# Optimization experiments

Hardware: AMD Instinct MI355X
Metric: run time of the kernel (lower is better)

## Reference

```python
import jax, jax.numpy as jnp
import numpy as np

N = 16384      # nodes
DEG = 20       # avg degree
E = N * DEG    # edges
MUL = 8        # multiplicity of 0e and 1o irreps
NB = 10        # number_of_basis
HID = 64       # fc hidden size
RMAX = 3.5     # max_radius
WNUM = 4 * MUL * MUL  # tp weight numel (4 parity-allowed paths)


def setup_inputs() -> dict:
    key = jax.random.key(0)
    ks = jax.random.split(key, 12)
    f = jax.random.normal(ks[0], (N, 4 * MUL), dtype=jnp.float32)  # 8 scalars + 8 vectors (3 comps)
    pos = jax.random.uniform(ks[1], (N, 3), dtype=jnp.float32) * 2.0  # box keeps dists < RMAX
    rng = np.random.default_rng(0)
    edge_dst = np.repeat(np.arange(N), DEG)
    edge_src = rng.integers(0, N, size=E)
    edge_src = np.where(edge_src == edge_dst, (edge_src + 1) % N, edge_src)
    return {
        'f': f, 'pos': pos,
        'Wq_s': jax.random.normal(ks[2], (MUL, MUL), jnp.float32),
        'Wq_v': jax.random.normal(ks[3], (MUL, MUL), jnp.float32),
        'Wk1': jax.random.normal(ks[4], (NB, HID), jnp.float32),
        'Wk2': jax.random.normal(ks[5], (HID, WNUM), jnp.float32),
        'Wv1': jax.random.normal(ks[6], (NB, HID), jnp.float32),
        'Wv2': jax.random.normal(ks[7], (HID, WNUM), jnp.float32),
        'Wd_s': jax.random.normal(ks[8], (MUL, MUL), jnp.float32),
        'Wd_v': jax.random.normal(ks[9], (MUL, MUL), jnp.float32),
        'edge_src': jnp.asarray(edge_src, jnp.int32),
        'edge_dst': jnp.asarray(edge_dst, jnp.int32),
    }


def _soft_unit_step(x):
    # e3nn soft_unit_step: exp(-1/x) for x>0 else 0; safe for grads
    xs = jnp.where(x > 0, x, 1.0)
    return jnp.where(x > 0, jnp.exp(-1.0 / xs), 0.0)


def _split(x):
    # [*, 4*MUL] -> scalars [*, MUL], vectors [*, MUL, 3]
    return x[:, :MUL], x[:, MUL:].reshape(-1, MUL, 3)


def _fc(x, W1, W2):
    # e3nn FullyConnectedNet: normalized linear -> act -> normalized linear
    h = jax.nn.silu(x @ W1 / jnp.sqrt(jnp.float32(NB)))
    return h @ W2 / jnp.sqrt(jnp.float32(HID))


def _tp(xs, xv, s0, s1, w):
    # fully connected tensor product (in: MULx0e+MULx1o) x (1x0e+1x1o) -> MULx0e+MULx1o
    # w: [E, 4, MUL, MUL]; paths: ss->s, vv->s (dot/sqrt3), sv->v, vs->v
    norm = 1.0 / (MUL ** 0.5 * 2.0 ** 0.5)
    out_s = (jnp.einsum('ei,eio->eo', xs * s0[:, None], w[:, 0]) +
             jnp.einsum('eic,ec,eio->eo', xv, s1, w[:, 1]) / 3.0 ** 0.5) * norm
    out_v = (jnp.einsum('ei,ec,eio->eoc', xs, s1, w[:, 2]) +
             jnp.einsum('eic,eio->eoc', xv * s0[:, None, None], w[:, 3])) * norm
    return out_s, out_v


def reference(f, pos, Wq_s, Wq_v, Wk1, Wk2, Wv1, Wv2, Wd_s, Wd_v, edge_src, edge_dst):
    edge_vec = pos[edge_src] - pos[edge_dst]                      # [E,3]
    r = jnp.linalg.norm(edge_vec, axis=1)                         # [E]
    # soft_one_hot_linspace, basis='smooth_finite', cutoff=True
    values = jnp.linspace(0.0, RMAX, NB + 2)[1:-1]
    step = RMAX / (NB + 1)
    d = (r[:, None] - values) / step
    basis = (1.14136 * np.exp(2.0)) * _soft_unit_step(d + 1.0) * _soft_unit_step(1.0 - d)
    emb = basis * NB ** 0.5                                       # [E,NB]
    cutoff = _soft_unit_step(10.0 * (1.0 - r / RMAX))             # [E]
    # spherical harmonics l=0,1; normalize=True, 'component' norm
    unit = edge_vec / r[:, None]
    s0 = jnp.ones_like(r)
    s1 = (3.0 ** 0.5) * unit                                      # [E,3]
    # query (equivariant linear per irrep)
    fs, fv = _split(f)
    qs = fs @ Wq_s / MUL ** 0.5                                   # [N,MUL]
    qv = jnp.einsum('eic,io->eoc', fv, Wq_v) / MUL ** 0.5         # [N,MUL,3]
    # per-edge tp weights from radial net
    wk = _fc(emb, Wk1, Wk2).reshape(E, 4, MUL, MUL)
    wv = _fc(emb, Wv1, Wv2).reshape(E, 4, MUL, MUL)
    gs, gv = fs[edge_src], fv[edge_src]                           # gather
    ks_, kv_ = _tp(gs, gv, s0, s1, wk)
    vs_, vv_ = _tp(gs, gv, s0, s1, wv)
    # dot tp (q x k -> 0e), shared weights
    qds, qdv = qs[edge_dst], qv[edge_dst]
    logits = (jnp.einsum('ei,ej,ij->e', qds, ks_, Wd_s) +
              jnp.einsum('eic,ejc,ij->e', qdv, kv_, Wd_v) / 3.0 ** 0.5) / (MUL * 2.0 ** 0.5)
    # scatter softmax with cutoff weighting
    mx = jax.ops.segment_max(logits, edge_dst, num_segments=N)
    mx = jnp.where(jnp.isneginf(mx), 0.0, mx)
    expw = cutoff * jnp.exp(logits - mx[edge_dst])
    z = jax.ops.segment_sum(expw, edge_dst, num_segments=N)
    z = jnp.where(z == 0, 1.0, z)
    alpha = expw / z[edge_dst]
    coef = jnp.sqrt(jax.nn.relu(alpha) + 1e-12)                   # [E]
    out_s = jax.ops.segment_sum(coef[:, None] * vs_, edge_dst, num_segments=N)
    out_v = jax.ops.segment_sum(coef[:, None, None] * vv_, edge_dst, num_segments=N)
    return jnp.concatenate([out_s, out_v.reshape(N, 3 * MUL)], axis=1)
```

## Files before the change

### kernel.cpp

```cpp
#include <hip/hip_runtime.h>
#include <hip/hip_bf16.h>
#include <math.h>

#define NN 16384
#define DEG 20
#define EE (NN*DEG)
#define RMAXF 3.5f
#define NGRP 5

typedef __attribute__((ext_vector_type(8))) short short8;
typedef __attribute__((ext_vector_type(4))) float f32x4;

__device__ __forceinline__ float su_f(float x) {
    return x > 0.0f ? __expf(-__builtin_amdgcn_rcpf(x)) : 0.0f;
}
__device__ __forceinline__ ushort f2bf(float x) {
    __hip_bfloat16 h = __float2bfloat16(x);
    return *reinterpret_cast<ushort*>(&h);
}
__device__ __forceinline__ float bf2f(ushort u) {
    return __uint_as_float(((unsigned int)u) << 16);
}

__global__ __launch_bounds__(256, 3) void edge_kernel(
    const float* __restrict__ f,   const float* __restrict__ pos,
    const float* __restrict__ Wqs, const float* __restrict__ Wqv,
    const float* __restrict__ Wds, const float* __restrict__ Wdv,
    const float* __restrict__ Wk1, const float* __restrict__ Wv1,
    const float* __restrict__ Wk2, const float* __restrict__ Wv2,
    const int* __restrict__ esrc,  float* __restrict__ out)
{
    __shared__ float  s_w[2][16][260];
    __shared__ __align__(16) ushort s_hb[2][16][64];
    __shared__ __align__(16) float s_g[2][16][36];
    __shared__ float s_emb[2][16][10];
    __shared__ float s_s1[2][16][4];
    __shared__ float s_b[16][9];
    __shared__ __align__(4) ushort s_v[80][34];
    __shared__ float s_lg[80];
    __shared__ float s_cut[80];
    __shared__ float s_mqn[4][32];
    __shared__ int   s_esrc[80];

    const int t = threadIdx.x;
    const int wave = t >> 6, lane = t & 63;
    const int qd = lane >> 4, n = lane & 15;
    const int n0 = blockIdx.x * 4;
    const int E0 = n0 * DEG;

    if (t < 128) {
        int nd = t >> 5, idx = t & 31;
        const float* fr = f + (size_t)(n0 + nd) * 32;
        const float inv8 = 0.35355339059327373f;
        float o_ = 0.0f;
        if (idx < 8) {
            int j = idx;
            #pragma unroll
            for (int i = 0; i < 8; i++) {
                float qs = 0.0f;
                #pragma unroll
                for (int a = 0; a < 8; a++) qs = fmaf(fr[a], Wqs[a * 8 + i], qs);
                o_ = fmaf(qs * inv8, Wds[i * 8 + j], o_);
            }
        } else {
            int kk = idx - 8;
            int j = kk / 3, c = kk - 3 * j;
            #pragma unroll
            for (int i = 0; i < 8; i++) {
                float qv = 0.0f;
                #pragma unroll
                for (int a = 0; a < 8; a++) qv = fmaf(fr[8 + 3 * a + c], Wqv[a * 8 + i], qv);
                o_ = fmaf(qv * inv8, Wdv[i * 8 + j], o_);
            }
            o_ *= 0.5773502691896258f;
        }
        s_mqn[nd][idx] = o_;
    }
    if (t < 80) s_esrc[t] = esrc[E0 + t];
    __syncthreads();

    float wk1r[10], wv1r[10];
    #pragma unroll
    for (int j = 0; j < 10; j++) {
        wk1r[j] = Wk1[j * 64 + lane];
        wv1r[j] = Wv1[j * 64 + lane];
    }

    short8 breg[2][2][4];
    #pragma unroll
    for (int net = 0; net < 2; net++) {
        const float* W2 = net ? Wv2 : Wk2;
        #pragma unroll
        for (int s = 0; s < 2; s++)
            #pragma unroll
            for (int jj = 0; jj < 4; jj++) {
                int col = (wave * 4 + jj) * 16 + n;
                union { ushort u[8]; short8 v; } bf;
                #pragma unroll
                for (int j = 0; j < 8; j++) {
                    int k0 = s * 32 + qd * 8 + j;
                    bf.u[j] = f2bf(W2[k0 * 256 + col] * 0.125f);
                }
                breg[net][s][jj] = bf.v;
            }
    }

    {
        int e = t >> 4, rl = t & 15;
        if (rl < 11) {
            int s = s_esrc[e];
            int d = n0;
            float vx = pos[s * 3 + 0] - pos[d * 3 + 0];
            float vy = pos[s * 3 + 1] - pos[d * 3 + 1];
            float vz = pos[s * 3 + 2] - pos[d * 3 + 2];
            float r = sqrtf(vx * vx + vy * vy + vz * vz);
            if (rl < 10) {
                const float step = RMAXF / 11.0f;
                const float invstep = 11.0f / RMAXF;
                const float K = 26.66929988626f;
                float dd = (r - step * (float)(rl + 1)) * invstep;
                s_emb[0][e][rl] = K * su_f(dd + 1.0f) * su_f(1.0f - dd);
            } else {
                float invr = __builtin_amdgcn_rcpf(r);
                const float sqrt3 = 1.7320508075688772f;
                s_s1[0][e][0] = sqrt3 * vx * invr;
                s_s1[0][e][1] = sqrt3 * vy * invr;
                s_s1[0][e][2] = sqrt3 * vz * invr;
                s_cut[e] = su_f(10.0f * (1.0f - r / RMAXF));
            }
        }
        if (t < 128) {
            int el = t >> 3, c4 = t & 7;
            int s = s_esrc[el];
            float4 x = *reinterpret_cast<const float4*>(f + (size_t)s * 32 + c4 * 4);
            *reinterpret_cast<float4*>(&s_g[0][el][c4 * 4]) = x;
        }
    }
    __syncthreads();

    for (int g = 0; g < NGRP; g++) {
        const int cb = g & 1, nbuf = cb ^ 1;
        const int le0 = g * 16;
        const bool more = (g + 1 < NGRP);

        float psx = 0.f, psy = 0.f, psz = 0.f, pdx = 0.f, pdy = 0.f, pdz = 0.f;
        float4 pf4 = {0.f, 0.f, 0.f, 0.f};
        {
            int e = t >> 4, rl = t & 15;
            if (more && rl < 11) {
                int s = s_esrc[le0 + 16 + e];
                int d = n0 + (le0 + 16 + e) / DEG;
                psx = pos[s * 3 + 0]; psy = pos[s * 3 + 1]; psz = pos[s * 3 + 2];
                pdx = pos[d * 3 + 0]; pdy = pos[d * 3 + 1]; pdz = pos[d * 3 + 2];
            }
            if (more && t < 128) {
                int el = t >> 3, c4 = t & 7;
                int s = s_esrc[le0 + 16 + el];
                pf4 = *reinterpret_cast<const float4*>(f + (size_t)s * 32 + c4 * 4);
            }
        }

        {
            const float invsq10 = 0.31622776601683794f;
            #pragma unroll
            for (int e = 0; e < 4; e++) {
                int el = wave * 4 + e;
                float ak = 0.0f, av = 0.0f;
                #pragma unroll
                for (int j = 0; j < 10; j++) {
                    float ej = s_emb[cb][el][j];
                    ak = fmaf(ej, wk1r[j], ak);
                    av = fmaf(ej, wv1r[j], av);
                }
                ak *= invsq10; av *= invsq10;
                float hk = ak * __builtin_amdgcn_rcpf(1.0f + __expf(-ak));
                float hv = av * __builtin_amdgcn_rcpf(1.0f + __expf(-av));
                int pos_ = ((((lane >> 3) ^ (el & 7))) << 3) | (lane & 7);
                s_hb[0][el][pos_] = f2bf(hk);
                s_hb[1][el][pos_] = f2bf(hv);
            }
            if (t < 128) {
                int el = t >> 3, k = t & 7;
                const float inv_sqrt3 = 0.5773502691896258f;
                s_b[el][k] = (s_g[cb][el][8 + 3 * k + 0] * s_s1[cb][el][0] +
                              s_g[cb][el][8 + 3 * k + 1] * s_s1[cb][el][1] +
                              s_g[cb][el][8 + 3 * k + 2] * s_s1[cb][el][2]) * inv_sqrt3;
            }
        }

        if (more) {
            int e = t >> 4, rl = t & 15;
            if (rl < 11) {
                float vx = psx - pdx, vy = psy - pdy, vz = psz - pdz;
                float r = sqrtf(vx * vx + vy * vy + vz * vz);
                if (rl < 10) {
                    const float step = RMAXF / 11.0f;
                    const float invstep = 11.0f / RMAXF;
                    const float K = 26.66929988626f;
                    float dd = (r - step * (float)(rl + 1)) * invstep;
                    s_emb[nbuf][e][rl] = K * su_f(dd + 1.0f) * su_f(1.0f - dd);
                } else {
                    float invr = __builtin_amdgcn_rcpf(r);
                    const float sqrt3 = 1.7320508075688772f;
                    s_s1[nbuf][e][0] = sqrt3 * vx * invr;
                    s_s1[nbuf][e][1] = sqrt3 * vy * invr;
                    s_s1[nbuf][e][2] = sqrt3 * vz * invr;
                    s_cut[le0 + 16 + e] = su_f(10.0f * (1.0f - r / RMAXF));
                }
            }
            if (t < 128) {
                int el = t >> 3, c4 = t & 7;
                *reinterpret_cast<float4*>(&s_g[nbuf][el][c4 * 4]) = pf4;
            }
        }
        __syncthreads();

        #pragma unroll
        for (int net = 0; net < 2; net++) {
            short8 ha0 = *(const short8*)&s_hb[net][n][((qd ^ (n & 7)) << 3)];
            short8 ha1 = *(const short8*)&s_hb[net][n][(((4 + qd) ^ (n & 7)) << 3)];
            #pragma unroll
            for (int jj = 0; jj < 4; jj++) {
                int tt = wave * 4 + jj;
                f32x4 d = {0.0f, 0.0f, 0.0f, 0.0f};
                d = __builtin_amdgcn_mfma_f32_16x16x32_bf16(ha0, breg[net][0][jj], d, 0, 0, 0);
                d = __builtin_amdgcn_mfma_f32_16x16x32_bf16(ha1, breg[net][1][jj], d, 0, 0, 0);
                #pragma unroll
                for (int r = 0; r < 4; r++)
                    s_w[net][4 * qd + r][tt * 16 + n] = d[r];
            }
        }
        __syncthreads();

        {
            int u = t & 127;
            int el = u >> 3, o = u & 7;
            int le = le0 + el;
            float g_[32];
            #pragma unroll
            for (int v4 = 0; v4 < 8; v4++) {
                float4 x = *reinterpret_cast<const float4*>(&s_g[cb][el][v4 * 4]);
                g_[v4 * 4 + 0] = x.x; g_[v4 * 4 + 1] = x.y;
                g_[v4 * 4 + 2] = x.z; g_[v4 * 4 + 3] = x.w;
            }
            const float nrm = 0.25f;

            if (t < 128) {
                int nd = le / DEG;
                const float* wk = s_w[0][el];
                float ks = 0.0f, uk = 0.0f;
                #pragma unroll
                for (int i = 0; i < 8; i++) {
                    ks += g_[i] * wk[i * 8 + o] + s_b[el][i] * wk[64 + i * 8 + o];
                    uk = fmaf(g_[i], wk[128 + i * 8 + o], uk);
                }
                float contrib = s_mqn[nd][o] * (ks * nrm);
                #pragma unroll
                for (int c = 0; c < 3; c++) {
                    float tk = 0.0f;
                    #pragma unroll
                    for (int i = 0; i < 8; i++)
                        tk = fmaf(g_[8 + 3 * i + c], wk[192 + i * 8 + o], tk);
                    float kv_c = nrm * (s_s1[cb][el][c] * uk + tk);
                    contrib = fmaf(s_mqn[nd][8 + 3 * o + c], kv_c, contrib);
                }
                contrib += __shfl_xor(contrib, 1);
                contrib += __shfl_xor(contrib, 2);
                contrib += __shfl_xor(contrib, 4);
                if (o == 0) s_lg[le] = contrib * 0.08838834764831845f;
            } else {
                const float* wv = s_w[1][el];
                float vs = 0.0f, uv = 0.0f;
                #pragma unroll
                for (int i = 0; i < 8; i++) {
                    vs += g_[i] * wv[i * 8 + o] + s_b[el][i] * wv[64 + i * 8 + o];
                    uv = fmaf(g_[i], wv[128 + i * 8 + o], uv);
                }
                s_v[le][o] = f2bf(vs * nrm);
                #pragma unroll
                for (int c = 0; c < 3; c++) {
                    float tv = 0.0f;
                    #pragma unroll
                    for (int i = 0; i < 8; i++)
                        tv = fmaf(g_[8 + 3 * i + c], wv[192 + i * 8 + o], tv);
                    s_v[le][8 + 3 * o + c] = f2bf(nrm * (s_s1[cb][el][c] * uv + tv));
                }
            }
        }
        __syncthreads();
    }

    {
        int base_le = DEG * wave;
        int h32 = lane & 32;
        int hl = lane & 31;
        float lg = -INFINITY, cw = 0.0f;
        if (hl < DEG) {
            lg = s_lg[base_le + hl];
            cw = s_cut[base_le + hl];
        }
        float mx = lg;
        mx = fmaxf(mx, __shfl_xor(mx, 16));
        mx = fmaxf(mx, __shfl_xor(mx, 8));
        mx = fmaxf(mx, __shfl_xor(mx, 4));
        mx = fmaxf(mx, __shfl_xor(mx, 2));
        mx = fmaxf(mx, __shfl_xor(mx, 1));

        float ew = cw * __expf(lg - mx);
        float z = ew;
        z += __shfl_xor(z, 16);
        z += __shfl_xor(z, 8);
        z += __shfl_xor(z, 4);
        z += __shfl_xor(z, 2);
        z += __shfl_xor(z, 1);
        z = (z == 0.0f) ? 1.0f : z;
        float coef = sqrtf(ew * __builtin_amdgcn_rcpf(z) + 1e-12f);

        float acc = 0.0f;
        #pragma unroll
        for (int ee = 0; ee < DEG; ee++) {
            float ce = __shfl(coef, h32 + ee);
            acc = fmaf(ce, bf2f(s_v[base_le + ee][hl]), acc);
        }
        if (lane < 32) out[(size_t)(n0 + wave) * 32 + hl] = acc;
    }
}

extern "C" void kernel_launch(void* const* d_in, const int* in_sizes, int n_in,
                              void* d_out, int out_size, void* d_ws, size_t ws_size,
                              hipStream_t stream) {
    const float* f    = (const float*)d_in[0];
    const float* pos  = (const float*)d_in[1];
    const float* Wqs  = (const float*)d_in[2];
    const float* Wqv  = (const float*)d_in[3];
    const float* Wk1  = (const float*)d_in[4];
    const float* Wk2  = (const float*)d_in[5];
    const float* Wv1  = (const float*)d_in[6];
    const float* Wv2  = (const float*)d_in[7];
    const float* Wds  = (const float*)d_in[8];
    const float* Wdv  = (const float*)d_in[9];
    const int* esrc   = (const int*)d_in[10];
    float* out        = (float*)d_out;

    edge_kernel<<<dim3(NN / 4), dim3(256), 0, stream>>>(
        f, pos, Wqs, Wqv, Wds, Wdv, Wk1, Wv1, Wk2, Wv2, esrc, out);
}
```

Baseline: 177.8 us.

## Deepen the edge-group software pipeline and drop one barrier per group

Result: slower. 195.4 us (+9.9%).

```diff
diff --git a/kernel.cpp b/kernel.cpp
--- a/kernel.cpp
+++ b/kernel.cpp
@@ -138,56 +138,64 @@
     }
     __syncthreads();
 
+    float psx = 0.f, psy = 0.f, psz = 0.f, pdx = 0.f, pdy = 0.f, pdz = 0.f;
+    float4 pf4 = {0.f, 0.f, 0.f, 0.f};
+    {
+        int e = t >> 4, rl = t & 15;
+        if (rl < 11) {
+            int s = s_esrc[16 + e];
+            int d = n0 + (16 + e) / DEG;
+            psx = pos[s * 3 + 0]; psy = pos[s * 3 + 1]; psz = pos[s * 3 + 2];
+            pdx = pos[d * 3 + 0]; pdy = pos[d * 3 + 1]; pdz = pos[d * 3 + 2];
+        }
+        if (t < 128) {
+            int el = t >> 3, c4 = t & 7;
+            int s = s_esrc[16 + el];
+            pf4 = *reinterpret_cast<const float4*>(f + (size_t)s * 32 + c4 * 4);
+        }
+    }
+    {
+        const float invsq10 = 0.31622776601683794f;
+        #pragma unroll
+        for (int e = 0; e < 4; e++) {
+            int el = wave * 4 + e;
+            float ak = 0.0f, av = 0.0f;
+            #pragma unroll
+            for (int j = 0; j < 10; j++) {
+                float ej = s_emb[0][el][j];
+                ak = fmaf(ej, wk1r[j], ak);
+                av = fmaf(ej, wv1r[j], av);
+            }
+            ak *= invsq10; av *= invsq10;
+            float hk = ak * __builtin_amdgcn_rcpf(1.0f + __expf(-ak));
+            float hv = av * __builtin_amdgcn_rcpf(1.0f + __expf(-av));
+            int pos_ = ((((lane >> 3) ^ (el & 7))) << 3) | (lane & 7);
+            s_hb[0][el][pos_] = f2bf(hk);
+            s_hb[1][el][pos_] = f2bf(hv);
+        }
+    }
+    __syncthreads();
+
     for (int g = 0; g < NGRP; g++) {
-        const int cb = g & 1, nbuf = cb ^ 1;
+        const int cb = g & 1, nb = cb ^ 1;
         const int le0 = g * 16;
         const bool more = (g + 1 < NGRP);
 
-        float psx = 0.f, psy = 0.f, psz = 0.f, pdx = 0.f, pdy = 0.f, pdz = 0.f;
-        float4 pf4 = {0.f, 0.f, 0.f, 0.f};
-        {
-            int e = t >> 4, rl = t & 15;
-            if (more && rl < 11) {
-                int s = s_esrc[le0 + 16 + e];
-                int d = n0 + (le0 + 16 + e) / DEG;
-                psx = pos[s * 3 + 0]; psy = pos[s * 3 + 1]; psz = pos[s * 3 + 2];
-                pdx = pos[d * 3 + 0]; pdy = pos[d * 3 + 1]; pdz = pos[d * 3 + 2];
-            }
-            if (more && t < 128) {
-                int el = t >> 3, c4 = t & 7;
-                int s = s_esrc[le0 + 16 + el];
-                pf4 = *reinterpret_cast<const float4*>(f + (size_t)s * 32 + c4 * 4);
-            }
-        }
-
-        {
-            const float invsq10 = 0.31622776601683794f;
-            #pragma unroll
-            for (int e = 0; e < 4; e++) {
-                int el = wave * 4 + e;
-                float ak = 0.0f, av = 0.0f;
-                #pragma unroll
-                for (int j = 0; j < 10; j++) {
-                    float ej = s_emb[cb][el][j];
-                    ak = fmaf(ej, wk1r[j], ak);
-                    av = fmaf(ej, wv1r[j], av);
-                }
-                ak *= invsq10; av *= invsq10;
-                float hk = ak * __builtin_amdgcn_rcpf(1.0f + __expf(-ak));
-                float hv = av * __builtin_amdgcn_rcpf(1.0f + __expf(-av));
-                int pos_ = ((((lane >> 3) ^ (el & 7))) << 3) | (lane & 7);
-                s_hb[0][el][pos_] = f2bf(hk);
-                s_hb[1][el][pos_] = f2bf(hv);
-            }
-            if (t < 128) {
-                int el = t >> 3, k = t & 7;
-                const float inv_sqrt3 = 0.5773502691896258f;
-                s_b[el][k] = (s_g[cb][el][8 + 3 * k + 0] * s_s1[cb][el][0] +
-                              s_g[cb][el][8 + 3 * k + 1] * s_s1[cb][el][1] +
-                              s_g[cb][el][8 + 3 * k + 2] * s_s1[cb][el][2]) * inv_sqrt3;
-            }
-        }
-
+        #pragma unroll
+        for (int net = 0; net < 2; net++) {
+            short8 ha0 = *(const short8*)&s_hb[net][n][((qd ^ (n & 7)) << 3)];
+            short8 ha1 = *(const short8*)&s_hb[net][n][(((4 + qd) ^ (n & 7)) << 3)];
+            #pragma unroll
+            for (int jj = 0; jj < 4; jj++) {
+                int tt = wave * 4 + jj;
+                f32x4 d = {0.0f, 0.0f, 0.0f, 0.0f};
+                d = __builtin_amdgcn_mfma_f32_16x16x32_bf16(ha0, breg[net][0][jj], d, 0, 0, 0);
+                d = __builtin_amdgcn_mfma_f32_16x16x32_bf16(ha1, breg[net][1][jj], d, 0, 0, 0);
+                #pragma unroll
+                for (int r = 0; r < 4; r++)
+                    s_w[net][4 * qd + r][tt * 16 + n] = d[r];
+            }
+        }
         if (more) {
             int e = t >> 4, rl = t & 15;
             if (rl < 11) {
@@ -198,40 +206,64 @@
                     const float invstep = 11.0f / RMAXF;
                     const float K = 26.66929988626f;
                     float dd = (r - step * (float)(rl + 1)) * invstep;
-                    s_emb[nbuf][e][rl] = K * su_f(dd + 1.0f) * su_f(1.0f - dd);
+                    s_emb[nb][e][rl] = K * su_f(dd + 1.0f) * su_f(1.0f - dd);
                 } else {
                     float invr = __builtin_amdgcn_rcpf(r);
                     const float sqrt3 = 1.7320508075688772f;
-                    s_s1[nbuf][e][0] = sqrt3 * vx * invr;
-                    s_s1[nbuf][e][1] = sqrt3 * vy * invr;
-                    s_s1[nbuf][e][2] = sqrt3 * vz * invr;
+                    s_s1[nb][e][0] = sqrt3 * vx * invr;
+                    s_s1[nb][e][1] = sqrt3 * vy * invr;
+                    s_s1[nb][e][2] = sqrt3 * vz * invr;
                     s_cut[le0 + 16 + e] = su_f(10.0f * (1.0f - r / RMAXF));
                 }
             }
             if (t < 128) {
                 int el = t >> 3, c4 = t & 7;
-                *reinterpret_cast<float4*>(&s_g[nbuf][el][c4 * 4]) = pf4;
-            }
+                *reinterpret_cast<float4*>(&s_g[nb][el][c4 * 4]) = pf4;
+            }
+        }
+        if (t < 128) {
+            int el = t >> 3, k = t & 7;
+            const float inv_sqrt3 = 0.5773502691896258f;
+            s_b[el][k] = (s_g[cb][el][8 + 3 * k + 0] * s_s1[cb][el][0] +
+                          s_g[cb][el][8 + 3 * k + 1] * s_s1[cb][el][1] +
+                          s_g[cb][el][8 + 3 * k + 2] * s_s1[cb][el][2]) * inv_sqrt3;
         }
         __syncthreads();
 
-        #pragma unroll
-        for (int net = 0; net < 2; net++) {
-            short8 ha0 = *(const short8*)&s_hb[net][n][((qd ^ (n & 7)) << 3)];
-            short8 ha1 = *(const short8*)&s_hb[net][n][(((4 + qd) ^ (n & 7)) << 3)];
-            #pragma unroll
-            for (int jj = 0; jj < 4; jj++) {
-                int tt = wave * 4 + jj;
-                f32x4 d = {0.0f, 0.0f, 0.0f, 0.0f};
-                d = __builtin_amdgcn_mfma_f32_16x16x32_bf16(ha0, breg[net][0][jj], d, 0, 0, 0);
-                d = __builtin_amdgcn_mfma_f32_16x16x32_bf16(ha1, breg[net][1][jj], d, 0, 0, 0);
-                #pragma unroll
-                for (int r = 0; r < 4; r++)
-                    s_w[net][4 * qd + r][tt * 16 + n] = d[r];
-            }
-        }
-        __syncthreads();
-
+        if (g + 2 < NGRP) {
+            int e = t >> 4, rl = t & 15;
+            if (rl < 11) {
+                int s = s_esrc[le0 + 32 + e];
+                int d = n0 + (le0 + 32 + e) / DEG;
+                psx = pos[s * 3 + 0]; psy = pos[s * 3 + 1]; psz = pos[s * 3 + 2];
+                pdx = pos[d * 3 + 0]; pdy = pos[d * 3 + 1]; pdz = pos[d * 3 + 2];
+            }
+            if (t < 128) {
+                int el = t >> 3, c4 = t & 7;
+                int s = s_esrc[le0 + 32 + el];
+                pf4 = *reinterpret_cast<const float4*>(f + (size_t)s * 32 + c4 * 4);
+            }
+        }
+        if (more) {
+            const float invsq10 = 0.31622776601683794f;
+            #pragma unroll
+            for (int e = 0; e < 4; e++) {
+                int el = wave * 4 + e;
+                float ak = 0.0f, av = 0.0f;
+                #pragma unroll
+                for (int j = 0; j < 10; j++) {
+                    float ej = s_emb[nb][el][j];
+                    ak = fmaf(ej, wk1r[j], ak);
+                    av = fmaf(ej, wv1r[j], av);
+                }
+                ak *= invsq10; av *= invsq10;
+                float hk = ak * __builtin_amdgcn_rcpf(1.0f + __expf(-ak));
+                float hv = av * __builtin_amdgcn_rcpf(1.0f + __expf(-av));
+                int pos_ = ((((lane >> 3) ^ (el & 7))) << 3) | (lane & 7);
+                s_hb[0][el][pos_] = f2bf(hk);
+                s_hb[1][el][pos_] = f2bf(hv);
+            }
+        }
         {
             int u = t & 127;
             int el = u >> 3, o = u & 7;
```
